# Kernel tuning notes

Measured on AMD Instinct MI355X. Metric: run time of the kernel, lower is better.

## Reference

```python
import jax, jax.numpy as jnp
import numpy as np

EPS = 1e-7  # K.epsilon()

_LC = np.zeros((3, 3, 3), np.float32)  # Levi-Civita for 1x1->1
_LC[0, 1, 2] = _LC[1, 2, 0] = _LC[2, 0, 1] = 1.0
_LC[0, 2, 1] = _LC[2, 1, 0] = _LC[1, 0, 2] = -1.0


def _ssp(x):
    # shifted softplus: log(0.5*exp(x)+0.5)
    return jnp.log(0.5 * jnp.exp(x) + 0.5)


def _radial(image, w1, b1, w2, b2):
    # Sequential([Dense(32), Dense(feat)]) -- linear Dense layers (no activation)
    return (image @ w1 + b1) @ w2 + b2  # (m, a, b, feat)


def setup_inputs() -> dict:
    key = jax.random.key(0)
    ks = jax.random.split(key, 16)
    M, A, RBF, F, SI, H = 4, 256, 64, 32, 32, 32
    inp = {}
    inp["image"] = jax.random.uniform(ks[0], (M, A, A, RBF), dtype=jnp.float32)
    inp["vectors"] = jax.random.normal(ks[1], (M, A, A, 3), dtype=jnp.float32)
    inp["feat0"] = jax.random.normal(ks[2], (M, A, F, 1), dtype=jnp.float32)
    inp["feat1"] = jax.random.normal(ks[3], (M, A, F, 3), dtype=jnp.float32)
    i = 4
    for rin in (0, 1):
        for fro in (0, 1):
            tag = f"{rin}{fro}"
            inp[f"w1_{tag}"] = jax.random.normal(ks[i], (RBF, H)) / np.sqrt(RBF).astype(np.float32)
            inp[f"b1_{tag}"] = jnp.zeros((H,), jnp.float32)
            i += 1
            inp[f"w2_{tag}"] = jax.random.normal(ks[i], (H, F)) / np.sqrt(np.float32(H))
            inp[f"b2_{tag}"] = jnp.zeros((F,), jnp.float32)
            i += 1
    inp["w_si0"] = jax.random.normal(ks[i], (SI, 2 * F)) / np.sqrt(np.float32(2 * F)); i += 1
    inp["w_si1"] = jax.random.normal(ks[i], (SI, 3 * F)) / np.sqrt(np.float32(3 * F)); i += 1
    inp["b_act0"] = jnp.zeros((SI,), jnp.float32)
    inp["b_act1"] = jnp.zeros((SI,), jnp.float32)
    return inp


def reference(image, vectors, feat0, feat1,
              w1_00, b1_00, w2_00, b2_00,
              w1_01, b1_01, w2_01, b2_01,
              w1_10, b1_10, w2_10, b2_10,
              w1_11, b1_11, w2_11, b2_11,
              w_si0, w_si1, b_act0, b_act1):
    # mask where |r_ab| < eps (self-pairs / padding)
    mask = (jnp.sqrt(jnp.sum(vectors * vectors, axis=-1)) < EPS)[..., None]  # (m,a,b,1)

    def filt0(w1, b1, w2, b2):
        return _radial(image, w1, b1, w2, b2)  # (m,a,b,F), implicit rep index of size 1

    def filt1(w1, b1, w2, b2):
        r = jnp.where(mask, 0.0, _radial(image, w1, b1, w2, b2))  # masked radial
        return vectors[:, :, :, None, :] * r[..., None]  # (m,a,b,F,3)

    f0_in0 = filt0(w1_00, b1_00, w2_00, b2_00)
    f1_in0 = filt1(w1_01, b1_01, w2_01, b2_01)
    f0_in1 = filt0(w1_10, b1_10, w2_10, b2_10)
    f1_in1 = filt1(w1_11, b1_11, w2_11, b2_11)

    # point convolution (sum over neighbor atoms b)
    out_0x0_0 = jnp.einsum('mabf,mbfj->mafj', f0_in0, feat0)   # (m,a,F,1)
    out_0x1_1 = jnp.einsum('mabfi,mbfj->mafi', f1_in0, feat0)  # (m,a,F,3)
    out_1x0_1 = jnp.einsum('mabf,mbfj->mafj', f0_in1, feat1)   # (m,a,F,3)
    cg0 = jnp.eye(3, dtype=image.dtype)[None]                  # (1,3,3): 1x1->0
    out_1x1_0 = jnp.einsum('ijk,mabfj,mbfk->mafi', cg0, f1_in1, feat1)  # (m,a,F,1)
    lc = jnp.asarray(_LC, image.dtype)                         # 1x1->1
    out_1x1_1 = jnp.einsum('ijk,mabfj,mbfk->mafi', lc, f1_in1, feat1)   # (m,a,F,3)

    # concat along channel dim per output RO
    cat0 = jnp.concatenate([out_0x0_0, out_1x1_0], axis=2)  # (m,a,2F,1)
    cat1 = jnp.concatenate([out_0x1_1, out_1x0_1, out_1x1_1], axis=2)  # (m,a,3F,3)

    # self-interaction: einsum('mafi,gf->maig') then transpose -> (m,a,g,i)
    si0 = jnp.einsum('mafi,gf->magi', cat0, w_si0)  # (m,a,SI,1)
    si1 = jnp.einsum('mafi,gf->magi', cat1, w_si1)  # (m,a,SI,3)

    # equivariant activation
    o0 = _ssp(si0 + b_act0[None, None, :, None])
    n1 = jnp.sqrt(jnp.maximum(jnp.sum(si1 * si1, axis=-1), EPS))  # norm_with_epsilon
    a1 = _ssp(n1 + b_act1)
    o1 = si1 * (a1 / n1)[..., None]
    return (o0, o1)
```

## Files before the change

### kernel.cpp

```cpp
#include <hip/hip_runtime.h>
#include <math.h>

#define M_ 4
#define A_ 256
#define RBF_ 64
#define F_ 32
#define H_ 32
#define SI_ 32
#define TF_ 128

typedef __attribute__((ext_vector_type(8))) short bf16x8;
typedef __attribute__((ext_vector_type(4))) float f32x4;

__device__ __forceinline__ unsigned short f2bf(float f) {
  union { float f; unsigned u; } v; v.f = f;
  unsigned r = v.u + 0x7FFFu + ((v.u >> 16) & 1u);
  return (unsigned short)(r >> 16);
}

__device__ __forceinline__ unsigned pack2bf(float lo, float hi) {
  union { float f; unsigned u; } a, b; a.f = lo; b.f = hi;
  return __builtin_amdgcn_perm(b.u + 0x8000u, a.u + 0x8000u, 0x07060302u);
}

__device__ __forceinline__ float sspf(float x) {
  return fmaxf(x, 0.f) + log1pf(expf(-fabsf(x))) - 0.6931471805599453f;
}

__global__ __launch_bounds__(256) void combine_weights(
    const float* __restrict__ w1_00, const float* __restrict__ b1_00,
    const float* __restrict__ w2_00, const float* __restrict__ b2_00,
    const float* __restrict__ w1_01, const float* __restrict__ b1_01,
    const float* __restrict__ w2_01, const float* __restrict__ b2_01,
    const float* __restrict__ w1_10, const float* __restrict__ b1_10,
    const float* __restrict__ w2_10, const float* __restrict__ b2_10,
    const float* __restrict__ w1_11, const float* __restrict__ b1_11,
    const float* __restrict__ w2_11, const float* __restrict__ b2_11,
    unsigned short* __restrict__ wsT, float* __restrict__ bcw)
{
  const float* w1s[4] = {w1_00, w1_01, w1_10, w1_11};
  const float* b1s[4] = {b1_00, b1_01, b1_10, b1_11};
  const float* w2s[4] = {w2_00, w2_01, w2_10, w2_11};
  const float* b2s[4] = {b2_00, b2_01, b2_10, b2_11};
  int tid = blockIdx.x * 256 + threadIdx.x;
  int k   = tid >> 7;
  int tf  = tid & 127;
  int tag = tf >> 5, f = tf & 31;
  const float* w1 = w1s[tag];
  const float* w2 = w2s[tag];
  float s = 0.f;
  for (int h = 0; h < H_; ++h) s += w1[k * H_ + h] * w2[h * F_ + f];
  wsT[tf * 64 + k] = f2bf(s);
  if (tid < TF_) {
    const float* b1 = b1s[tag];
    const float* b2 = b2s[tag];
    float sb = b2[f];
    for (int h = 0; h < H_; ++h) sb += b1[h] * w2[h * F_ + f];
    bcw[tf] = sb;
  }
}

__global__ __launch_bounds__(256, 4) void conv_main(
    const float* __restrict__ image, const float* __restrict__ vectors,
    const float* __restrict__ feat0, const float* __restrict__ feat1,
    const unsigned short* __restrict__ wsT, const float* __restrict__ bcw,
    const float* __restrict__ w_si0, const float* __restrict__ w_si1,
    const float* __restrict__ b_act0, const float* __restrict__ b_act1,
    float* __restrict__ out)
{
  __shared__ __align__(16) char smem[36864];
  unsigned short* sA  = (unsigned short*)smem;
  float*          red = (float*)smem;

  const int t    = threadIdx.x;
  const int m    = blockIdx.x >> 8;
  const int a    = blockIdx.x & 255;
  const int w    = t >> 6;
  const int l    = t & 63;
  const int n    = l & 15;
  const int quad = l >> 4;
  const int which   = w & 1;
  const int pairsel = ((w >> 1) ^ blockIdx.x) & 1;
  const int tagA = pairsel ? 1 : 0;
  const int tagB = pairsel ? 2 : 3;
  const int ctA  = tagA * 2 + which;
  const int ctB  = tagB * 2 + which;
  const int f    = which * 16 + n;

  const unsigned short* wrA = wsT + (ctA * 16 + n) * 64 + quad * 8;
  const unsigned short* wrB = wsT + (ctB * 16 + n) * 64 + quad * 8;
  const bf16x8 wA0 = *(const bf16x8*)(wrA);
  const bf16x8 wA1 = *(const bf16x8*)(wrA + 32);
  const bf16x8 wB0 = *(const bf16x8*)(wrB);
  const bf16x8 wB1 = *(const bf16x8*)(wrB + 32);
  const float  bcA = bcw[ctA * 16 + n];
  const float  bcB = bcw[ctB * 16 + n];

  const float* imgMA = image + ((size_t)(m * A_ + a)) * A_ * RBF_;
  #pragma unroll
  for (int i = 0; i < 8; ++i) {
    int g = t + 256 * i;
    int r = g >> 3, c8 = g & 7;
    const float* src = imgMA + r * RBF_ + c8 * 8;
    float4 v0 = *(const float4*)(src);
    float4 v1 = *(const float4*)(src + 4);
    uint4 pk;
    pk.x = pack2bf(v0.x, v0.y);
    pk.y = pack2bf(v0.z, v0.w);
    pk.z = pack2bf(v1.x, v1.y);
    pk.w = pack2bf(v1.z, v1.w);
    *(uint4*)&sA[r * 72 + c8 * 8] = pk;
  }

  const float* p0 = feat0 + (size_t)(m * A_) * F_ + f;
  const float* p1 = feat1 + ((size_t)(m * A_) * F_ + f) * 3;
  const float* pv = vectors + ((size_t)(m * A_ + a)) * A_ * 3;

  float ft0[2][4], gg[2][3][4], vv[2][3][4];
  float pS0 = 0.f, pS1 = 0.f, pV0 = 0.f, pV1 = 0.f, pV2 = 0.f;
  float pW0 = 0.f, pW1 = 0.f, pW2 = 0.f;

#define PF(BUF, BT) { \
    const int b0 = (BT) * 16 + quad * 4; \
    _Pragma("unroll") \
    for (int r = 0; r < 4; ++r) { \
      ft0[BUF][r] = p0[(b0 + r) * F_]; \
      const float* fp = p1 + (size_t)(b0 + r) * (F_ * 3); \
      gg[BUF][0][r] = fp[0]; gg[BUF][1][r] = fp[1]; gg[BUF][2][r] = fp[2]; \
      const float* vp = pv + (b0 + r) * 3; \
      vv[BUF][0][r] = vp[0]; vv[BUF][1][r] = vp[1]; vv[BUF][2][r] = vp[2]; \
    } }

#define BODY(BT, BUF) { \
    const int brow = (BT) * 16; \
    const bf16x8 a0 = *(const bf16x8*)&sA[(brow + n) * 72 + quad * 8]; \
    const bf16x8 a1 = *(const bf16x8*)&sA[(brow + n) * 72 + 32 + quad * 8]; \
    f32x4 accA = {bcA, bcA, bcA, bcA}; \
    f32x4 accB = {bcB, bcB, bcB, bcB}; \
    accA = __builtin_amdgcn_mfma_f32_16x16x32_bf16(a0, wA0, accA, 0, 0, 0); \
    accA = __builtin_amdgcn_mfma_f32_16x16x32_bf16(a1, wA1, accA, 0, 0, 0); \
    accB = __builtin_amdgcn_mfma_f32_16x16x32_bf16(a0, wB0, accB, 0, 0, 0); \
    accB = __builtin_amdgcn_mfma_f32_16x16x32_bf16(a1, wB1, accB, 0, 0, 0); \
    if (pairsel == 0) {             \
      _Pragma("unroll") \
      for (int r = 0; r < 4; ++r) pS0 += accA[r] * ft0[BUF][r]; \
      _Pragma("unroll") \
      for (int r = 0; r < 4; ++r) { \
        const float Rr = accB[r]; \
        const float gx = gg[BUF][0][r], gy = gg[BUF][1][r], gz = gg[BUF][2][r]; \
        const float ux = vv[BUF][0][r], uy = vv[BUF][1][r], uz = vv[BUF][2][r]; \
        pS1 += Rr * (ux * gx + uy * gy + uz * gz); \
        pV0 += Rr * (uy * gz - uz * gy); \
        pV1 += Rr * (uz * gx - ux * gz); \
        pV2 += Rr * (ux * gy - uy * gx); \
      } \
    } else {                        \
      _Pragma("unroll") \
      for (int r = 0; r < 4; ++r) { \
        const float s = accA[r] * ft0[BUF][r]; \
        pV0 += vv[BUF][0][r] * s; \
        pV1 += vv[BUF][1][r] * s; \
        pV2 += vv[BUF][2][r] * s; \
        const float Rb = accB[r]; \
        pW0 += Rb * gg[BUF][0][r]; \
        pW1 += Rb * gg[BUF][1][r]; \
        pW2 += Rb * gg[BUF][2][r]; \
      } \
    } }

  PF(0, 0)
  __syncthreads();

  #pragma unroll 1
  for (int bth = 0; bth < 8; ++bth) {
    const int bt0 = bth * 2;
    PF(1, bt0 + 1)
    BODY(bt0, 0)
    if (bth < 7) PF(0, bt0 + 2)
    BODY(bt0 + 1, 1)
  }

  __syncthreads();

  if (pairsel == 0) {
    red[f * 5 + quad]                 = pS0;
    red[(32 + f) * 5 + quad]          = pS1;
    red[(256 + f * 3 + 0) * 5 + quad] = pV0;
    red[(256 + f * 3 + 1) * 5 + quad] = pV1;
    red[(256 + f * 3 + 2) * 5 + quad] = pV2;
  } else {
    red[(64 + f * 3 + 0) * 5 + quad]  = pV0;
    red[(64 + f * 3 + 1) * 5 + quad]  = pV1;
    red[(64 + f * 3 + 2) * 5 + quad]  = pV2;
    red[(160 + f * 3 + 0) * 5 + quad] = pW0;
    red[(160 + f * 3 + 1) * 5 + quad] = pW1;
    red[(160 + f * 3 + 2) * 5 + quad] = pW2;
  }
  __syncthreads();

  for (int s = t; s < 352; s += 256)
    red[s * 5 + 4] = red[s * 5 + 0] + red[s * 5 + 1] +
                     red[s * 5 + 2] + red[s * 5 + 3];
  __syncthreads();

  const int outBase = (m * A_ + a) * SI_;
  if (t < 32) {
    const float* wr = w_si0 + t * 64;
    float s = 0.f;
    #pragma unroll 8
    for (int ff = 0; ff < 64; ++ff) s += red[ff * 5 + 4] * wr[ff];
    s += b_act0[t];
    out[outBase + t] = sspf(s);
  } else if (t >= 64 && t < 96) {
    int g = t - 64;
    const float* wr = w_si1 + g * 96;
    float s0 = 0.f, s1 = 0.f, s2 = 0.f;
    #pragma unroll 8
    for (int ff = 0; ff < 96; ++ff) {
      float wv = wr[ff];
      s0 += red[(64 + ff * 3 + 0) * 5 + 4] * wv;
      s1 += red[(64 + ff * 3 + 1) * 5 + 4] * wv;
      s2 += red[(64 + ff * 3 + 2) * 5 + 4] * wv;
    }
    float n2 = s0 * s0 + s1 * s1 + s2 * s2;
    float n1 = sqrtf(fmaxf(n2, 1e-7f));
    float a1 = sspf(n1 + b_act1[g]);
    float sc = a1 / n1;
    int ob = M_ * A_ * SI_ + (outBase + g) * 3;
    out[ob + 0] = s0 * sc;
    out[ob + 1] = s1 * sc;
    out[ob + 2] = s2 * sc;
  }
}

extern "C" void kernel_launch(void* const* d_in, const int* in_sizes, int n_in,
                              void* d_out, int out_size, void* d_ws, size_t ws_size,
                              hipStream_t stream) {
  const float* image   = (const float*)d_in[0];
  const float* vectors = (const float*)d_in[1];
  const float* feat0   = (const float*)d_in[2];
  const float* feat1   = (const float*)d_in[3];
  const float* w_si0   = (const float*)d_in[20];
  const float* w_si1   = (const float*)d_in[21];
  const float* b_act0  = (const float*)d_in[22];
  const float* b_act1  = (const float*)d_in[23];
  unsigned short* wsT = (unsigned short*)d_ws;
  float* bcw = (float*)((char*)d_ws + 16384);
  float* out = (float*)d_out;

  combine_weights<<<32, 256, 0, stream>>>(
      (const float*)d_in[4],  (const float*)d_in[5],
      (const float*)d_in[6],  (const float*)d_in[7],
      (const float*)d_in[8],  (const float*)d_in[9],
      (const float*)d_in[10], (const float*)d_in[11],
      (const float*)d_in[12], (const float*)d_in[13],
      (const float*)d_in[14], (const float*)d_in[15],
      (const float*)d_in[16], (const float*)d_in[17],
      (const float*)d_in[18], (const float*)d_in[19],
      wsT, bcw);

  conv_main<<<M_ * A_, 256, 0, stream>>>(
      image, vectors, feat0, feat1, wsT, bcw,
      w_si0, w_si1, b_act0, b_act1, out);
}
```

Baseline: 178.3 us.

## Split neighbor range across two blocks and move self-interaction to separate epilogue kernel

The main convolution kernel now splits each (m,a) row's 256 neighbors into two halves handled by separate blocks. This doubles the grid, halves per-block shared memory, and raises the occupancy hint. Quad partial sums are reduced with wave shuffles instead of a shared-memory reduction, and each half writes 352 partials to workspace. A new small kernel sums the two halves and applies the self-interaction and activation, which adds a launch and a global round-trip of partials.

```diff
diff --git a/kernel.cpp b/kernel.cpp
--- a/kernel.cpp
+++ b/kernel.cpp
@@ -60,27 +60,25 @@
   }
 }
 
-__global__ __launch_bounds__(256, 4) void conv_main(
+__global__ __launch_bounds__(256, 8) void conv_partial(
     const float* __restrict__ image, const float* __restrict__ vectors,
     const float* __restrict__ feat0, const float* __restrict__ feat1,
     const unsigned short* __restrict__ wsT, const float* __restrict__ bcw,
-    const float* __restrict__ w_si0, const float* __restrict__ w_si1,
-    const float* __restrict__ b_act0, const float* __restrict__ b_act1,
-    float* __restrict__ out)
+    float* __restrict__ part)
 {
-  __shared__ __align__(16) char smem[36864];
-  unsigned short* sA  = (unsigned short*)smem;
-  float*          red = (float*)smem;
+  __shared__ __align__(16) unsigned short sA[128 * 72];
 
   const int t    = threadIdx.x;
-  const int m    = blockIdx.x >> 8;
-  const int a    = blockIdx.x & 255;
+  const int bid  = blockIdx.x;
+  const int ma   = bid >> 1;
+  const int half = bid & 1;
+  const int m    = ma >> 8;
   const int w    = t >> 6;
   const int l    = t & 63;
   const int n    = l & 15;
   const int quad = l >> 4;
   const int which   = w & 1;
-  const int pairsel = ((w >> 1) ^ blockIdx.x) & 1;
+  const int pairsel = ((w >> 1) ^ bid) & 1;
   const int tagA = pairsel ? 1 : 0;
   const int tagB = pairsel ? 2 : 3;
   const int ctA  = tagA * 2 + which;
@@ -96,12 +94,12 @@
   const float  bcA = bcw[ctA * 16 + n];
   const float  bcB = bcw[ctB * 16 + n];
 
-  const float* imgMA = image + ((size_t)(m * A_ + a)) * A_ * RBF_;
+  const float* imgH = image + ((size_t)ma * A_ + half * 128) * RBF_;
   #pragma unroll
-  for (int i = 0; i < 8; ++i) {
+  for (int i = 0; i < 4; ++i) {
     int g = t + 256 * i;
     int r = g >> 3, c8 = g & 7;
-    const float* src = imgMA + r * RBF_ + c8 * 8;
+    const float* src = imgH + r * RBF_ + c8 * 8;
     float4 v0 = *(const float4*)(src);
     float4 v1 = *(const float4*)(src + 4);
     uint4 pk;
@@ -114,14 +112,14 @@
 
   const float* p0 = feat0 + (size_t)(m * A_) * F_ + f;
   const float* p1 = feat1 + ((size_t)(m * A_) * F_ + f) * 3;
-  const float* pv = vectors + ((size_t)(m * A_ + a)) * A_ * 3;
+  const float* pv = vectors + (size_t)ma * A_ * 3;
 
   float ft0[2][4], gg[2][3][4], vv[2][3][4];
   float pS0 = 0.f, pS1 = 0.f, pV0 = 0.f, pV1 = 0.f, pV2 = 0.f;
   float pW0 = 0.f, pW1 = 0.f, pW2 = 0.f;
 
 #define PF(BUF, BT) { \
-    const int b0 = (BT) * 16 + quad * 4; \
+    const int b0 = half * 128 + (BT) * 16 + quad * 4; \
     _Pragma("unroll") \
     for (int r = 0; r < 4; ++r) { \
       ft0[BUF][r] = p0[(b0 + r) * F_]; \
@@ -172,55 +170,70 @@
   __syncthreads();
 
   #pragma unroll 1
-  for (int bth = 0; bth < 8; ++bth) {
+  for (int bth = 0; bth < 4; ++bth) {
     const int bt0 = bth * 2;
     PF(1, bt0 + 1)
     BODY(bt0, 0)
-    if (bth < 7) PF(0, bt0 + 2)
+    if (bth < 3) PF(0, bt0 + 2)
     BODY(bt0 + 1, 1)
   }
 
+#define QRED(x) { x += __shfl_xor(x, 16); x += __shfl_xor(x, 32); }
+  float* dst = part + ((size_t)ma * 2 + half) * 352;
+  if (pairsel == 0) {
+    QRED(pS0) QRED(pS1) QRED(pV0) QRED(pV1) QRED(pV2)
+    if (quad == 0) {
+      dst[f]                 = pS0;
+      dst[32 + f]            = pS1;
+      dst[256 + f * 3 + 0]   = pV0;
+      dst[256 + f * 3 + 1]   = pV1;
+      dst[256 + f * 3 + 2]   = pV2;
+    }
+  } else {
+    QRED(pV0) QRED(pV1) QRED(pV2) QRED(pW0) QRED(pW1) QRED(pW2)
+    if (quad == 0) {
+      dst[64 + f * 3 + 0]    = pV0;
+      dst[64 + f * 3 + 1]    = pV1;
+      dst[64 + f * 3 + 2]    = pV2;
+      dst[160 + f * 3 + 0]   = pW0;
+      dst[160 + f * 3 + 1]   = pW1;
+      dst[160 + f * 3 + 2]   = pW2;
+    }
+  }
+}
+
+__global__ __launch_bounds__(64) void si_epilogue(
+    const float* __restrict__ part,
+    const float* __restrict__ w_si0, const float* __restrict__ w_si1,
+    const float* __restrict__ b_act0, const float* __restrict__ b_act1,
+    float* __restrict__ out)
+{
+  __shared__ float cat[352];
+  const int ma = blockIdx.x;
+  const int t  = threadIdx.x;
+  const float* pA = part + (size_t)ma * 704;
+  const float* pB = pA + 352;
+  for (int s = t; s < 352; s += 64) cat[s] = pA[s] + pB[s];
   __syncthreads();
 
-  if (pairsel == 0) {
-    red[f * 5 + quad]                 = pS0;
-    red[(32 + f) * 5 + quad]          = pS1;
-    red[(256 + f * 3 + 0) * 5 + quad] = pV0;
-    red[(256 + f * 3 + 1) * 5 + quad] = pV1;
-    red[(256 + f * 3 + 2) * 5 + quad] = pV2;
-  } else {
-    red[(64 + f * 3 + 0) * 5 + quad]  = pV0;
-    red[(64 + f * 3 + 1) * 5 + quad]  = pV1;
-    red[(64 + f * 3 + 2) * 5 + quad]  = pV2;
-    red[(160 + f * 3 + 0) * 5 + quad] = pW0;
-    red[(160 + f * 3 + 1) * 5 + quad] = pW1;
-    red[(160 + f * 3 + 2) * 5 + quad] = pW2;
-  }
-  __syncthreads();
-
-  for (int s = t; s < 352; s += 256)
-    red[s * 5 + 4] = red[s * 5 + 0] + red[s * 5 + 1] +
-                     red[s * 5 + 2] + red[s * 5 + 3];
-  __syncthreads();
-
-  const int outBase = (m * A_ + a) * SI_;
+  const int outBase = ma * SI_;
   if (t < 32) {
     const float* wr = w_si0 + t * 64;
     float s = 0.f;
     #pragma unroll 8
-    for (int ff = 0; ff < 64; ++ff) s += red[ff * 5 + 4] * wr[ff];
+    for (int ff = 0; ff < 64; ++ff) s += cat[ff] * wr[ff];
     s += b_act0[t];
     out[outBase + t] = sspf(s);
-  } else if (t >= 64 && t < 96) {
-    int g = t - 64;
+  } else {
+    int g = t - 32;
     const float* wr = w_si1 + g * 96;
     float s0 = 0.f, s1 = 0.f, s2 = 0.f;
     #pragma unroll 8
     for (int ff = 0; ff < 96; ++ff) {
       float wv = wr[ff];
-      s0 += red[(64 + ff * 3 + 0) * 5 + 4] * wv;
-      s1 += red[(64 + ff * 3 + 1) * 5 + 4] * wv;
-      s2 += red[(64 + ff * 3 + 2) * 5 + 4] * wv;
+      s0 += cat[64 + ff * 3 + 0] * wv;
+      s1 += cat[64 + ff * 3 + 1] * wv;
+      s2 += cat[64 + ff * 3 + 2] * wv;
     }
     float n2 = s0 * s0 + s1 * s1 + s2 * s2;
     float n1 = sqrtf(fmaxf(n2, 1e-7f));
@@ -245,8 +258,9 @@
   const float* b_act0  = (const float*)d_in[22];
   const float* b_act1  = (const float*)d_in[23];
   unsigned short* wsT = (unsigned short*)d_ws;
-  float* bcw = (float*)((char*)d_ws + 16384);
-  float* out = (float*)d_out;
+  float* bcw  = (float*)((char*)d_ws + 16384);
+  float* part = (float*)((char*)d_ws + 32768);
+  float* out  = (float*)d_out;
 
   combine_weights<<<32, 256, 0, stream>>>(
       (const float*)d_in[4],  (const float*)d_in[5],
@@ -259,7 +273,9 @@
       (const float*)d_in[18], (const float*)d_in[19],
       wsT, bcw);
 
-  conv_main<<<M_ * A_, 256, 0, stream>>>(
-      image, vectors, feat0, feat1, wsT, bcw,
-      w_si0, w_si1, b_act0, b_act1, out);
-}
+  conv_partial<<<2 * M_ * A_, 256, 0, stream>>>(
+      image, vectors, feat0, feat1, wsT, bcw, part);
+
+  si_epilogue<<<M_ * A_, 64, 0, stream>>>(
+      part, w_si0, w_si1, b_act0, b_act1, out);
+}
```

Measured after the change: 470.8 us. 2.64x slower.

## Split filter tags across eight waves with 512-thread blocks and shuffle reduction

Applied to the files above, without the earlier changes.

Doubles the block to 512 threads so each wave computes one (tag, half-F) filter tile with a single MFMA pair instead of two. Each wave now does tag-specific contraction work with a wave-uniform branch. The per-block vectors row is staged into LDS, and only the needed feat0/feat1 data is loaded per tag. The quad partial sums are reduced with cross-lane shuffles instead of an LDS pass. This spreads the image-staging and MFMA work over more waves to raise parallelism, at the cost of higher per-block resource use and LDS reads of vectors inside the inner loop.

```diff
diff --git a/kernel.cpp b/kernel.cpp
--- a/kernel.cpp
+++ b/kernel.cpp
@@ -11,6 +11,7 @@
 
 typedef __attribute__((ext_vector_type(8))) short bf16x8;
 typedef __attribute__((ext_vector_type(4))) float f32x4;
+typedef __attribute__((ext_vector_type(3))) float f32x3;
 
 __device__ __forceinline__ unsigned short f2bf(float f) {
   union { float f; unsigned u; } v; v.f = f;
@@ -60,7 +61,7 @@
   }
 }
 
-__global__ __launch_bounds__(256, 4) void conv_main(
+__global__ __launch_bounds__(512, 4) void conv_main(
     const float* __restrict__ image, const float* __restrict__ vectors,
     const float* __restrict__ feat0, const float* __restrict__ feat1,
     const unsigned short* __restrict__ wsT, const float* __restrict__ bcw,
@@ -68,38 +69,32 @@
     const float* __restrict__ b_act0, const float* __restrict__ b_act1,
     float* __restrict__ out)
 {
-  __shared__ __align__(16) char smem[36864];
+  __shared__ __align__(16) char smem[39936];
   unsigned short* sA  = (unsigned short*)smem;
-  float*          red = (float*)smem;
+  float*          sV  = (float*)(smem + 36864);
+  float*          cat = (float*)smem;
 
   const int t    = threadIdx.x;
-  const int m    = blockIdx.x >> 8;
-  const int a    = blockIdx.x & 255;
-  const int w    = t >> 6;
+  const int ma   = blockIdx.x;
+  const int m    = ma >> 8;
   const int l    = t & 63;
   const int n    = l & 15;
   const int quad = l >> 4;
-  const int which   = w & 1;
-  const int pairsel = ((w >> 1) ^ blockIdx.x) & 1;
-  const int tagA = pairsel ? 1 : 0;
-  const int tagB = pairsel ? 2 : 3;
-  const int ctA  = tagA * 2 + which;
-  const int ctB  = tagB * 2 + which;
-  const int f    = which * 16 + n;
-
-  const unsigned short* wrA = wsT + (ctA * 16 + n) * 64 + quad * 8;
-  const unsigned short* wrB = wsT + (ctB * 16 + n) * 64 + quad * 8;
-  const bf16x8 wA0 = *(const bf16x8*)(wrA);
-  const bf16x8 wA1 = *(const bf16x8*)(wrA + 32);
-  const bf16x8 wB0 = *(const bf16x8*)(wrB);
-  const bf16x8 wB1 = *(const bf16x8*)(wrB + 32);
-  const float  bcA = bcw[ctA * 16 + n];
-  const float  bcB = bcw[ctB * 16 + n];
-
-  const float* imgMA = image + ((size_t)(m * A_ + a)) * A_ * RBF_;
+  const int wu    = __builtin_amdgcn_readfirstlane(t >> 6);
+  const int which = wu & 1;
+  const int tag   = wu >> 1;
+  const int ct    = tag * 2 + which;
+  const int f     = which * 16 + n;
+
+  const unsigned short* wr = wsT + (ct * 16 + n) * 64 + quad * 8;
+  const bf16x8 w0 = *(const bf16x8*)(wr);
+  const bf16x8 w1 = *(const bf16x8*)(wr + 32);
+  const float  bc = bcw[ct * 16 + n];
+
+  const float* imgMA = image + (size_t)ma * A_ * RBF_;
   #pragma unroll
-  for (int i = 0; i < 8; ++i) {
-    int g = t + 256 * i;
+  for (int i = 0; i < 4; ++i) {
+    int g = t + 512 * i;
     int r = g >> 3, c8 = g & 7;
     const float* src = imgMA + r * RBF_ + c8 * 8;
     float4 v0 = *(const float4*)(src);
@@ -111,60 +106,68 @@
     pk.w = pack2bf(v1.z, v1.w);
     *(uint4*)&sA[r * 72 + c8 * 8] = pk;
   }
+  #pragma unroll
+  for (int i = 0; i < 2; ++i) {
+    int s = t + 512 * i;
+    if (s < 768) sV[s] = vectors[(size_t)ma * (A_ * 3) + s];
+  }
 
   const float* p0 = feat0 + (size_t)(m * A_) * F_ + f;
   const float* p1 = feat1 + ((size_t)(m * A_) * F_ + f) * 3;
-  const float* pv = vectors + ((size_t)(m * A_ + a)) * A_ * 3;
-
-  float ft0[2][4], gg[2][3][4], vv[2][3][4];
-  float pS0 = 0.f, pS1 = 0.f, pV0 = 0.f, pV1 = 0.f, pV2 = 0.f;
-  float pW0 = 0.f, pW1 = 0.f, pW2 = 0.f;
+
+  float gx[2][4], gy[2][4], gz[2][4];
+  float pA = 0.f, pB0 = 0.f, pB1 = 0.f, pB2 = 0.f;
 
 #define PF(BUF, BT) { \
     const int b0 = (BT) * 16 + quad * 4; \
-    _Pragma("unroll") \
-    for (int r = 0; r < 4; ++r) { \
-      ft0[BUF][r] = p0[(b0 + r) * F_]; \
-      const float* fp = p1 + (size_t)(b0 + r) * (F_ * 3); \
-      gg[BUF][0][r] = fp[0]; gg[BUF][1][r] = fp[1]; gg[BUF][2][r] = fp[2]; \
-      const float* vp = pv + (b0 + r) * 3; \
-      vv[BUF][0][r] = vp[0]; vv[BUF][1][r] = vp[1]; vv[BUF][2][r] = vp[2]; \
+    if (tag <= 1) { \
+      _Pragma("unroll") \
+      for (int r = 0; r < 4; ++r) gx[BUF][r] = p0[(b0 + r) * F_]; \
+    } else { \
+      _Pragma("unroll") \
+      for (int r = 0; r < 4; ++r) { \
+        f32x3 v = *(const f32x3*)&p1[(size_t)(b0 + r) * (F_ * 3)]; \
+        gx[BUF][r] = v[0]; gy[BUF][r] = v[1]; gz[BUF][r] = v[2]; \
+      } \
     } }
 
 #define BODY(BT, BUF) { \
     const int brow = (BT) * 16; \
+    const int lb   = brow + quad * 4; \
     const bf16x8 a0 = *(const bf16x8*)&sA[(brow + n) * 72 + quad * 8]; \
     const bf16x8 a1 = *(const bf16x8*)&sA[(brow + n) * 72 + 32 + quad * 8]; \
-    f32x4 accA = {bcA, bcA, bcA, bcA}; \
-    f32x4 accB = {bcB, bcB, bcB, bcB}; \
-    accA = __builtin_amdgcn_mfma_f32_16x16x32_bf16(a0, wA0, accA, 0, 0, 0); \
-    accA = __builtin_amdgcn_mfma_f32_16x16x32_bf16(a1, wA1, accA, 0, 0, 0); \
-    accB = __builtin_amdgcn_mfma_f32_16x16x32_bf16(a0, wB0, accB, 0, 0, 0); \
-    accB = __builtin_amdgcn_mfma_f32_16x16x32_bf16(a1, wB1, accB, 0, 0, 0); \
-    if (pairsel == 0) {             \
-      _Pragma("unroll") \
-      for (int r = 0; r < 4; ++r) pS0 += accA[r] * ft0[BUF][r]; \
-      _Pragma("unroll") \
-      for (int r = 0; r < 4; ++r) { \
-        const float Rr = accB[r]; \
-        const float gx = gg[BUF][0][r], gy = gg[BUF][1][r], gz = gg[BUF][2][r]; \
-        const float ux = vv[BUF][0][r], uy = vv[BUF][1][r], uz = vv[BUF][2][r]; \
-        pS1 += Rr * (ux * gx + uy * gy + uz * gz); \
-        pV0 += Rr * (uy * gz - uz * gy); \
-        pV1 += Rr * (uz * gx - ux * gz); \
-        pV2 += Rr * (ux * gy - uy * gx); \
-      } \
-    } else {                        \
-      _Pragma("unroll") \
-      for (int r = 0; r < 4; ++r) { \
-        const float s = accA[r] * ft0[BUF][r]; \
-        pV0 += vv[BUF][0][r] * s; \
-        pV1 += vv[BUF][1][r] * s; \
-        pV2 += vv[BUF][2][r] * s; \
-        const float Rb = accB[r]; \
-        pW0 += Rb * gg[BUF][0][r]; \
-        pW1 += Rb * gg[BUF][1][r]; \
-        pW2 += Rb * gg[BUF][2][r]; \
+    f32x4 acc = {bc, bc, bc, bc}; \
+    acc = __builtin_amdgcn_mfma_f32_16x16x32_bf16(a0, w0, acc, 0, 0, 0); \
+    acc = __builtin_amdgcn_mfma_f32_16x16x32_bf16(a1, w1, acc, 0, 0, 0); \
+    if (tag == 0) {             \
+      _Pragma("unroll") \
+      for (int r = 0; r < 4; ++r) pA += acc[r] * gx[BUF][r]; \
+    } else if (tag == 1) {      \
+      _Pragma("unroll") \
+      for (int r = 0; r < 4; ++r) { \
+        const float s  = acc[r] * gx[BUF][r]; \
+        pB0 += sV[(lb + r) * 3 + 0] * s; \
+        pB1 += sV[(lb + r) * 3 + 1] * s; \
+        pB2 += sV[(lb + r) * 3 + 2] * s; \
+      } \
+    } else if (tag == 2) {      \
+      _Pragma("unroll") \
+      for (int r = 0; r < 4; ++r) { \
+        const float Rr = acc[r]; \
+        pB0 += Rr * gx[BUF][r]; pB1 += Rr * gy[BUF][r]; pB2 += Rr * gz[BUF][r]; \
+      } \
+    } else {                    \
+      _Pragma("unroll") \
+      for (int r = 0; r < 4; ++r) { \
+        const float Rr = acc[r]; \
+        const float ax = gx[BUF][r], ay = gy[BUF][r], az = gz[BUF][r]; \
+        const float vx = sV[(lb + r) * 3 + 0]; \
+        const float vy = sV[(lb + r) * 3 + 1]; \
+        const float vz = sV[(lb + r) * 3 + 2]; \
+        pA  += Rr * (vx * ax + vy * ay + vz * az); \
+        pB0 += Rr * (vy * az - vz * ay); \
+        pB1 += Rr * (vz * ax - vx * az); \
+        pB2 += Rr * (vx * ay - vy * ax); \
       } \
     } }
 
@@ -180,47 +183,48 @@
     BODY(bt0 + 1, 1)
   }
 
+#define QRED(x) { x += __shfl_xor(x, 16); x += __shfl_xor(x, 32); }
+  QRED(pA) QRED(pB0) QRED(pB1) QRED(pB2)
+
   __syncthreads();
-
-  if (pairsel == 0) {
-    red[f * 5 + quad]                 = pS0;
-    red[(32 + f) * 5 + quad]          = pS1;
-    red[(256 + f * 3 + 0) * 5 + quad] = pV0;
-    red[(256 + f * 3 + 1) * 5 + quad] = pV1;
-    red[(256 + f * 3 + 2) * 5 + quad] = pV2;
-  } else {
-    red[(64 + f * 3 + 0) * 5 + quad]  = pV0;
-    red[(64 + f * 3 + 1) * 5 + quad]  = pV1;
-    red[(64 + f * 3 + 2) * 5 + quad]  = pV2;
-    red[(160 + f * 3 + 0) * 5 + quad] = pW0;
-    red[(160 + f * 3 + 1) * 5 + quad] = pW1;
-    red[(160 + f * 3 + 2) * 5 + quad] = pW2;
+  if (quad == 0) {
+    if (tag == 0) {
+      cat[f] = pA;
+    } else if (tag == 1) {
+      cat[64 + f * 3 + 0] = pB0;
+      cat[64 + f * 3 + 1] = pB1;
+      cat[64 + f * 3 + 2] = pB2;
+    } else if (tag == 2) {
+      cat[160 + f * 3 + 0] = pB0;
+      cat[160 + f * 3 + 1] = pB1;
+      cat[160 + f * 3 + 2] = pB2;
+    } else {
+      cat[32 + f] = pA;
+      cat[256 + f * 3 + 0] = pB0;
+      cat[256 + f * 3 + 1] = pB1;
+      cat[256 + f * 3 + 2] = pB2;
+    }
   }
   __syncthreads();
 
-  for (int s = t; s < 352; s += 256)
-    red[s * 5 + 4] = red[s * 5 + 0] + red[s * 5 + 1] +
-                     red[s * 5 + 2] + red[s * 5 + 3];
-  __syncthreads();
-
-  const int outBase = (m * A_ + a) * SI_;
+  const int outBase = ma * SI_;
   if (t < 32) {
-    const float* wr = w_si0 + t * 64;
+    const float* wsr = w_si0 + t * 64;
     float s = 0.f;
     #pragma unroll 8
-    for (int ff = 0; ff < 64; ++ff) s += red[ff * 5 + 4] * wr[ff];
+    for (int ff = 0; ff < 64; ++ff) s += cat[ff] * wsr[ff];
     s += b_act0[t];
     out[outBase + t] = sspf(s);
-  } else if (t >= 64 && t < 96) {
-    int g = t - 64;
-    const float* wr = w_si1 + g * 96;
+  } else if (t < 64) {
+    int g = t - 32;
+    const float* wsr = w_si1 + g * 96;
     float s0 = 0.f, s1 = 0.f, s2 = 0.f;
     #pragma unroll 8
     for (int ff = 0; ff < 96; ++ff) {
-      float wv = wr[ff];
-      s0 += red[(64 + ff * 3 + 0) * 5 + 4] * wv;
-      s1 += red[(64 + ff * 3 + 1) * 5 + 4] * wv;
-      s2 += red[(64 + ff * 3 + 2) * 5 + 4] * wv;
+      float wv = wsr[ff];
+      s0 += cat[64 + ff * 3 + 0] * wv;
+      s1 += cat[64 + ff * 3 + 1] * wv;
+      s2 += cat[64 + ff * 3 + 2] * wv;
     }
     float n2 = s0 * s0 + s1 * s1 + s2 * s2;
     float n1 = sqrtf(fmaxf(n2, 1e-7f));
@@ -245,8 +249,8 @@
   const float* b_act0  = (const float*)d_in[22];
   const float* b_act1  = (const float*)d_in[23];
   unsigned short* wsT = (unsigned short*)d_ws;
-  float* bcw = (float*)((char*)d_ws + 16384);
-  float* out = (float*)d_out;
+  float* bcw  = (float*)((char*)d_ws + 16384);
+  float* out  = (float*)d_out;
 
   combine_weights<<<32, 256, 0, stream>>>(
       (const float*)d_in[4],  (const float*)d_in[5],
@@ -259,7 +263,7 @@
       (const float*)d_in[18], (const float*)d_in[19],
       wsT, bcw);
 
-  conv_main<<<M_ * A_, 256, 0, stream>>>(
+  conv_main<<<M_ * A_, 512, 0, stream>>>(
       image, vectors, feat0, feat1, wsT, bcw,
       w_si0, w_si1, b_act0, b_act1, out);
 }
```

Result: faster. 167.2 us (-6.2%).
